# Kernel optimization log

Hardware: AMD Instinct MI355X
Metric: run time of the kernel (lower is better)

Reference implementation:

```python
import jax, jax.numpy as jnp
import numpy as np

B, T, C = 2, 4096, 768
N_HEAD = 12
HEAD_DIM = C // N_HEAD


def setup_inputs() -> dict:
    key = jax.random.key(0)
    k1, k2, k3, k4, k5 = jax.random.split(key, 5)
    scale = 1.0 / np.sqrt(C)
    x = jax.random.normal(k1, (B, T, C), dtype=jnp.float32)
    # weights stored as [in, out] (transpose of torch Linear weight)
    W_attn = jax.random.normal(k2, (C, 3 * C), dtype=jnp.float32) * scale
    b_attn = jax.random.normal(k3, (3 * C,), dtype=jnp.float32) * 0.01
    W_proj = jax.random.normal(k4, (C, C), dtype=jnp.float32) * scale
    b_proj = jax.random.normal(k5, (C,), dtype=jnp.float32) * 0.01
    return {"x": x, "W_attn": W_attn, "b_attn": b_attn, "W_proj": W_proj, "b_proj": b_proj}


def reference(x, W_attn, b_attn, W_proj, b_proj):
    Bq, Tq, Cq = x.shape
    qkv = x @ W_attn + b_attn                      # [B, T, 3C]
    q, k, v = jnp.split(qkv, 3, axis=-1)           # each [B, T, C]

    def heads(t):
        return t.reshape(Bq, Tq, N_HEAD, HEAD_DIM).transpose(0, 2, 1, 3)  # [B, H, T, D]

    q, k, v = heads(q), heads(k), heads(v)
    att = jnp.einsum('bhqd,bhkd->bhqk', q, k) * (1.0 / np.sqrt(HEAD_DIM))  # [B, H, T, T]
    causal = jnp.tril(jnp.ones((Tq, Tq), dtype=bool))                      # [T, T]
    att = jnp.where(causal[None, None], att, jnp.finfo(att.dtype).min)
    att = jax.nn.softmax(att, axis=-1)
    y = jnp.einsum('bhqk,bhkd->bhqd', att, v)      # [B, H, T, D]
    y = y.transpose(0, 2, 1, 3).reshape(Bq, Tq, Cq)
    return y @ W_proj + b_proj
```

## Files before the change

kernel.cpp:

```cpp
#include <hip/hip_runtime.h>


#define TSEQ   4096
#define NHEAD  12
#define CDIM   768
#define C3     2304
#define BT_TOT 8192

#define PSTR   72

typedef __bf16 bf16x8 __attribute__((ext_vector_type(8)));
typedef __bf16 bf16x2 __attribute__((ext_vector_type(2)));
typedef float  f32x4  __attribute__((ext_vector_type(4)));

__device__ __forceinline__ unsigned short f2bf(float f) {
  unsigned int u = __builtin_bit_cast(unsigned int, f);
  u += 0x7FFFu + ((u >> 16) & 1u);
  return (unsigned short)(u >> 16);
}

__device__ __forceinline__ unsigned int pack2bf(float a, float b) {
  bf16x2 v = {(__bf16)a, (__bf16)b};
  return __builtin_bit_cast(unsigned int, v);
}

__device__ __forceinline__ f32x4 mfma16(bf16x8 a, bf16x8 b, f32x4 c) {
  return __builtin_amdgcn_mfma_f32_16x16x32_bf16(a, b, c, 0, 0, 0);
}

typedef const __attribute__((address_space(1))) void* gas_ptr;
typedef __attribute__((address_space(3))) void* las_ptr;

#define LGKM_WAIT() __builtin_amdgcn_s_waitcnt(0xC07F)


__global__ __launch_bounds__(256) void cast_f32_bf16(const float* __restrict__ x,
                                                     unsigned short* __restrict__ o, int n) {
  int i = (blockIdx.x * 256 + threadIdx.x) * 4;
  if (i < n) {
    float4 v = *(const float4*)(x + i);
    ushort4 u;
    u.x = f2bf(v.x); u.y = f2bf(v.y); u.z = f2bf(v.z); u.w = f2bf(v.w);
    *(ushort4*)(o + i) = u;
  }
}

__global__ __launch_bounds__(256) void transpose_cast(const float* __restrict__ src,
                                                      unsigned short* __restrict__ dst,
                                                      int K, int N) {
  __shared__ float tile[32][33];
  int n0 = blockIdx.x * 32, k0 = blockIdx.y * 32;
  int tx = threadIdx.x, ty = threadIdx.y;
#pragma unroll
  for (int i = 0; i < 4; ++i)
    tile[ty + i * 8][tx] = src[(size_t)(k0 + ty + i * 8) * N + n0 + tx];
  __syncthreads();
#pragma unroll
  for (int i = 0; i < 4; ++i)
    dst[(size_t)(n0 + ty + i * 8) * K + k0 + tx] = f2bf(tile[tx][ty + i * 8]);
}


__device__ __forceinline__ void gemm_bt_mainloop(const unsigned short* __restrict__ A,
                                                 const unsigned short* __restrict__ BTm,
                                                 int K, int m0, int n0,
                                                 unsigned short* lds, f32x4 acc[4][4]) {
  const int tid = threadIdx.x;
  const int wave = tid >> 6, lane = tid & 63;
  const int quad = lane >> 4, l16 = lane & 15;
  const int wm = (wave >> 1) * 64, wn = (wave & 1) * 64;
  const int srow = tid >> 2;
  const int scol = (tid & 3) * 8;

  for (int k0 = 0; k0 < K; k0 += 32) {
    __syncthreads();
#pragma unroll
    for (int r = 0; r < 2; ++r) {
      const unsigned short* ga = A + (size_t)(m0 + r * 64 + srow) * K + k0 + scol;
      __builtin_amdgcn_global_load_lds((gas_ptr)ga,
          (las_ptr)(lds + r * 2048 + wave * 512), 16, 0, 0);
      const unsigned short* gb = BTm + (size_t)(n0 + r * 64 + srow) * K + k0 + scol;
      __builtin_amdgcn_global_load_lds((gas_ptr)gb,
          (las_ptr)(lds + 4096 + r * 2048 + wave * 512), 16, 0, 0);
    }
    __syncthreads();

    bf16x8 af[4], bfr[4];
#pragma unroll
    for (int i = 0; i < 4; ++i) {
      af[i]  = *(const bf16x8*)(lds + (wm + i * 16 + l16) * 32 + quad * 8);
      bfr[i] = *(const bf16x8*)(lds + 4096 + (wn + i * 16 + l16) * 32 + quad * 8);
    }
#pragma unroll
    for (int i = 0; i < 4; ++i)
#pragma unroll
      for (int j = 0; j < 4; ++j)
        acc[i][j] = mfma16(af[i], bfr[j], acc[i][j]);
  }
}

__global__ __launch_bounds__(256) void gemm_qkv_kernel(
    const unsigned short* __restrict__ A, const unsigned short* __restrict__ BTm,
    const float* __restrict__ bias,
    unsigned short* __restrict__ qbuf, unsigned short* __restrict__ kbuf,
    unsigned short* __restrict__ vtbuf) {
  __shared__ __align__(16) unsigned short lds[128 * 136];
  f32x4 zero = {0.f, 0.f, 0.f, 0.f};
  f32x4 acc[4][4];
#pragma unroll
  for (int i = 0; i < 4; ++i)
#pragma unroll
    for (int j = 0; j < 4; ++j) acc[i][j] = zero;

  const int m0 = blockIdx.y * 128, n0 = blockIdx.x * 128;
  gemm_bt_mainloop(A, BTm, CDIM, m0, n0, lds, acc);

  const int tid = threadIdx.x;
  const int wave = tid >> 6, lane = tid & 63;
  const int quad = lane >> 4, l16 = lane & 15;
  const int wm = (wave >> 1) * 64, wn = (wave & 1) * 64;
  const float KSCALE = 0.125f * 1.44269504088896340736f;

  const int seg = n0 / CDIM;
  const float mult = (seg == 1) ? KSCALE : 1.0f;

  __syncthreads();
#pragma unroll
  for (int j = 0; j < 4; ++j) {
    const int nl = wn + j * 16 + l16;
    const float bv = bias[n0 + nl];
#pragma unroll
    for (int i = 0; i < 4; ++i) {
#pragma unroll
      for (int r = 0; r < 4; ++r) {
        const int ml = wm + i * 16 + quad * 4 + r;
        unsigned short val = f2bf((acc[i][j][r] + bv) * mult);
        if (seg < 2) lds[ml * 136 + nl] = val;
        else         lds[nl * 136 + ml] = val;
      }
    }
  }
  __syncthreads();

  const int row = tid >> 1, half = tid & 1;
  const unsigned short* src = lds + row * 136 + half * 64;
  unsigned short* dst;
  if (seg < 2) {
    const int m = m0 + row, b = m >> 12, t = m & (TSEQ - 1);
    const int nn = (n0 - seg * CDIM) + half * 64;
    const int h = nn >> 6;
    unsigned short* base = (seg == 0) ? qbuf : kbuf;
    dst = base + ((size_t)(b * NHEAD + h) * TSEQ + t) * 64;
  } else {
    const int nn = (n0 - 2 * CDIM) + row;
    const int h = nn >> 6, d = nn & 63;
    const int b = m0 >> 12, t0 = (m0 & (TSEQ - 1)) + half * 64;
    dst = vtbuf + ((size_t)(b * NHEAD + h) * 64 + d) * TSEQ + t0;
  }
#pragma unroll
  for (int k = 0; k < 8; ++k)
    *(uint4*)(dst + k * 8) = *(const uint4*)(src + k * 8);
}

__global__ __launch_bounds__(256) void gemm_out_kernel(
    const unsigned short* __restrict__ A, const unsigned short* __restrict__ BTm,
    const float* __restrict__ bias, float* __restrict__ out) {
  __shared__ __align__(16) unsigned short lds[8192];
  f32x4 zero = {0.f, 0.f, 0.f, 0.f};
  f32x4 acc[4][4];
#pragma unroll
  for (int i = 0; i < 4; ++i)
#pragma unroll
    for (int j = 0; j < 4; ++j) acc[i][j] = zero;

  const int m0 = blockIdx.y * 128, n0 = blockIdx.x * 128;
  gemm_bt_mainloop(A, BTm, CDIM, m0, n0, lds, acc);

  const int tid = threadIdx.x;
  const int wave = tid >> 6, lane = tid & 63;
  const int quad = lane >> 4, l16 = lane & 15;
  const int wm = (wave >> 1) * 64, wn = (wave & 1) * 64;

#pragma unroll
  for (int j = 0; j < 4; ++j) {
    int n = n0 + wn + j * 16 + l16;
    float bv = bias[n];
#pragma unroll
    for (int i = 0; i < 4; ++i) {
#pragma unroll
      for (int r = 0; r < 4; ++r) {
        int m = m0 + wm + i * 16 + quad * 4 + r;
        out[(size_t)m * CDIM + n] = acc[i][j][r] + bv;
      }
    }
  }
}


__device__ __forceinline__ void stage_kv4(const unsigned short* __restrict__ Kp,
                                          const unsigned short* __restrict__ Vp,
                                          int j0, unsigned short* kb, unsigned short* vb,
                                          int tid, int wave) {
  const int row = tid >> 3;
  const int col = ((tid & 7) ^ (row & 7)) * 8;
  __builtin_amdgcn_global_load_lds((gas_ptr)(Kp + (size_t)(j0 + row) * 64 + col),
                                   (las_ptr)(kb + wave * 512), 16, 0, 0);
  __builtin_amdgcn_global_load_lds((gas_ptr)(Kp + (size_t)(j0 + 32 + row) * 64 + col),
                                   (las_ptr)(kb + 2048 + wave * 512), 16, 0, 0);
  __builtin_amdgcn_global_load_lds((gas_ptr)(Vp + (size_t)row * TSEQ + j0 + col),
                                   (las_ptr)(vb + wave * 512), 16, 0, 0);
  __builtin_amdgcn_global_load_lds((gas_ptr)(Vp + (size_t)(row + 32) * TSEQ + j0 + col),
                                   (las_ptr)(vb + 2048 + wave * 512), 16, 0, 0);
}

__device__ __forceinline__ void qk_score(const bf16x8 kf[8], const bf16x8 qf[2], f32x4 s[4]) {
  f32x4 zero = {0.f, 0.f, 0.f, 0.f};
#pragma unroll
  for (int i = 0; i < 4; ++i)
    s[i] = mfma16(kf[2 * i + 1], qf[1], mfma16(kf[2 * i], qf[0], zero));
}

template <bool MASKED>
__device__ __forceinline__ void exp_write(const f32x4 s[4], unsigned short* __restrict__ prow,
                                          int j0, int q0, int l16, int quad, float& lsum) {
#pragma unroll
  for (int i = 0; i < 4; ++i) {
    float p[4];
#pragma unroll
    for (int r = 0; r < 4; ++r) {
      p[r] = __builtin_amdgcn_exp2f(s[i][r]);
      if (MASKED) {
        if (j0 + i * 16 + quad * 4 + r > q0 + l16) p[r] = 0.f;
      }
      lsum += p[r];
    }
    uint2 w;
    w.x = pack2bf(p[0], p[1]);
    w.y = pack2bf(p[2], p[3]);
    *(uint2*)(prow + l16 * PSTR + i * 16 + quad * 4) = w;
  }
}

__device__ __forceinline__ void pv8(const unsigned short* __restrict__ vb, int kcol0,
                                    const unsigned short* __restrict__ prow,
                                    int l16, int quad, f32x4 o[4]) {
  bf16x8 pf0 = *(const bf16x8*)(prow + l16 * PSTR + quad * 8);
  bf16x8 pf1 = *(const bf16x8*)(prow + l16 * PSTR + 32 + quad * 8);
#pragma unroll
  for (int dt = 0; dt < 4; ++dt) {
    bf16x8 v0 = *(const bf16x8*)(vb + (16 * dt + l16) * 64 + kcol0);
    bf16x8 v1 = *(const bf16x8*)(vb + (16 * dt + l16) * 64 + (kcol0 ^ 32));
    o[dt] = mfma16(pf1, v1, mfma16(pf0, v0, o[dt]));
  }
}

__global__ __launch_bounds__(256, 3) void attn_kernel(const unsigned short* __restrict__ qbuf,
                                                      const unsigned short* __restrict__ kbuf,
                                                      const unsigned short* __restrict__ vtbuf,
                                                      unsigned short* __restrict__ y) {
  __shared__ __align__(16) unsigned short k_lds[2][64 * 64];
  __shared__ __align__(16) unsigned short v_lds[2][64 * 64];
  __shared__ __align__(16) unsigned short p_lds[4][2][16 * PSTR];

  const int tid = threadIdx.x;
  const int wave = tid >> 6, lane = tid & 63;
  const int quad = lane >> 4, l16 = lane & 15;

  const int bh = blockIdx.x % 24;
  const int p = blockIdx.x / 24;
  const int qA0 = p * 64 + wave * 16;
  const int qB0 = (63 - p) * 64 + wave * 16;

  const unsigned short* Qp = qbuf + (size_t)bh * TSEQ * 64;
  const unsigned short* Kp = kbuf + (size_t)bh * TSEQ * 64;
  const unsigned short* Vp = vtbuf + (size_t)bh * 64 * TSEQ;
  unsigned short* prowA = &p_lds[wave][0][0];
  unsigned short* prowB = &p_lds[wave][1][0];

  bf16x8 qfA[2], qfB[2];
  qfA[0] = *(const bf16x8*)(Qp + (size_t)(qA0 + l16) * 64 + quad * 8);
  qfA[1] = *(const bf16x8*)(Qp + (size_t)(qA0 + l16) * 64 + 32 + quad * 8);
  qfB[0] = *(const bf16x8*)(Qp + (size_t)(qB0 + l16) * 64 + quad * 8);
  qfB[1] = *(const bf16x8*)(Qp + (size_t)(qB0 + l16) * 64 + 32 + quad * 8);

  f32x4 zero = {0.f, 0.f, 0.f, 0.f};
  f32x4 oA[4], oB[4];
#pragma unroll
  for (int dt = 0; dt < 4; ++dt) { oA[dt] = zero; oB[dt] = zero; }
  float lsA = 0.f, lsB = 0.f;

  const int kcol0 = (quad ^ (l16 & 7)) * 8;
  const int ntiles = 64 - p;

  stage_kv4(Kp, Vp, 0, k_lds[0], v_lds[0], tid, wave);

  for (int jt = 0; jt < ntiles; ++jt) {
    __syncthreads();
    if (jt + 1 < ntiles)
      stage_kv4(Kp, Vp, (jt + 1) * 64, k_lds[(jt + 1) & 1], v_lds[(jt + 1) & 1], tid, wave);

    const unsigned short* kb = k_lds[jt & 1];
    const unsigned short* vb = v_lds[jt & 1];
    const int j0 = jt * 64;
    const bool actA = jt <= p;

    bf16x8 kf[8];
#pragma unroll
    for (int i = 0; i < 4; ++i) {
      kf[2 * i]     = *(const bf16x8*)(kb + (16 * i + l16) * 64 + kcol0);
      kf[2 * i + 1] = *(const bf16x8*)(kb + (16 * i + l16) * 64 + (kcol0 ^ 32));
    }

    f32x4 sA[4], sB[4];
    if (actA) {
      qk_score(kf, qfA, sA);
      if (jt == p) exp_write<true>(sA, prowA, j0, qA0, l16, quad, lsA);
      else         exp_write<false>(sA, prowA, j0, qA0, l16, quad, lsA);
    }
    qk_score(kf, qfB, sB);
    if (jt == ntiles - 1) exp_write<true>(sB, prowB, j0, qB0, l16, quad, lsB);
    else                  exp_write<false>(sB, prowB, j0, qB0, l16, quad, lsB);

    LGKM_WAIT();

    if (actA) pv8(vb, kcol0, prowA, l16, quad, oA);
    pv8(vb, kcol0, prowB, l16, quad, oB);
  }

  lsA += __shfl_xor(lsA, 16); lsA += __shfl_xor(lsA, 32);
  lsB += __shfl_xor(lsB, 16); lsB += __shfl_xor(lsB, 32);

  const int b = bh / NHEAD, h = bh - b * NHEAD;
#pragma unroll
  for (int r = 0; r < 4; ++r) {
    const int qrow = quad * 4 + r;
    float lqA = __shfl(lsA, (lane & 48) + qrow);
    float lqB = __shfl(lsB, (lane & 48) + qrow);
    float invA = 1.0f / lqA, invB = 1.0f / lqB;
    size_t rowA = (size_t)(b * TSEQ + qA0 + qrow) * CDIM + h * 64;
    size_t rowB = (size_t)(b * TSEQ + qB0 + qrow) * CDIM + h * 64;
#pragma unroll
    for (int dt = 0; dt < 4; ++dt) {
      y[rowA + dt * 16 + l16] = f2bf(oA[dt][r] * invA);
      y[rowB + dt * 16 + l16] = f2bf(oB[dt][r] * invB);
    }
  }
}


extern "C" void kernel_launch(void* const* d_in, const int* in_sizes, int n_in,
                              void* d_out, int out_size, void* d_ws, size_t ws_size,
                              hipStream_t stream) {
  const float* x      = (const float*)d_in[0];
  const float* W_attn = (const float*)d_in[1];
  const float* b_attn = (const float*)d_in[2];
  const float* W_proj = (const float*)d_in[3];
  const float* b_proj = (const float*)d_in[4];
  float* out = (float*)d_out;

  unsigned short* xb    = (unsigned short*)d_ws;
  unsigned short* WaT   = xb + (size_t)BT_TOT * CDIM;
  unsigned short* WpT   = WaT + (size_t)C3 * CDIM;
  unsigned short* qbuf  = WpT + (size_t)CDIM * CDIM;
  unsigned short* kbuf  = qbuf + (size_t)2 * NHEAD * TSEQ * 64;
  unsigned short* vtbuf = kbuf + (size_t)2 * NHEAD * TSEQ * 64;
  unsigned short* ybuf  = xb;

  cast_f32_bf16<<<(BT_TOT * CDIM) / 1024, 256, 0, stream>>>(x, xb, BT_TOT * CDIM);
  transpose_cast<<<dim3(C3 / 32, CDIM / 32), dim3(32, 8), 0, stream>>>(W_attn, WaT, CDIM, C3);
  transpose_cast<<<dim3(CDIM / 32, CDIM / 32), dim3(32, 8), 0, stream>>>(W_proj, WpT, CDIM, CDIM);

  gemm_qkv_kernel<<<dim3(C3 / 128, BT_TOT / 128), 256, 0, stream>>>(xb, WaT, b_attn,
                                                                    qbuf, kbuf, vtbuf);
  attn_kernel<<<dim3(24 * 32), 256, 0, stream>>>(qbuf, kbuf, vtbuf, ybuf);
  gemm_out_kernel<<<dim3(CDIM / 128, BT_TOT / 128), 256, 0, stream>>>(ybuf, WpT, b_proj, out);
}
```

Measured before the change: 241.4 us.

## Use 64-wide K tiles with XOR swizzle in GEMMs; compute softmax row sums via MFMA

The shared GEMM mainloop now stages 64-element K slices with an XOR-swizzled LDS layout and runs two MFMA sub-steps per barrier pair. This halves the number of synchronizations per tile and avoids LDS bank conflicts, at the cost of doubling LDS use in the output GEMM. In attention, the per-lane scalar accumulation of softmax row sums and the shuffle reduction are replaced by an MFMA against a ones vector on the bf16 P tile. V fragments are also loaded once per tile and shared by both query halves. The row sums are now taken from bf16-rounded probabilities, which slightly changes the normalization.

```diff
diff --git a/kernel.cpp b/kernel.cpp
--- a/kernel.cpp
+++ b/kernel.cpp
@@ -61,41 +61,44 @@
 }
 
 
-__device__ __forceinline__ void gemm_bt_mainloop(const unsigned short* __restrict__ A,
-                                                 const unsigned short* __restrict__ BTm,
-                                                 int K, int m0, int n0,
-                                                 unsigned short* lds, f32x4 acc[4][4]) {
+__device__ __forceinline__ void gemm_bt_mainloop64(const unsigned short* __restrict__ A,
+                                                   const unsigned short* __restrict__ BTm,
+                                                   int K, int m0, int n0,
+                                                   unsigned short* lds, f32x4 acc[4][4]) {
   const int tid = threadIdx.x;
   const int wave = tid >> 6, lane = tid & 63;
   const int quad = lane >> 4, l16 = lane & 15;
   const int wm = (wave >> 1) * 64, wn = (wave & 1) * 64;
-  const int srow = tid >> 2;
-  const int scol = (tid & 3) * 8;
-
-  for (int k0 = 0; k0 < K; k0 += 32) {
+  const int srow = lane >> 3;
+  const int scol = ((lane & 7) ^ srow) * 8;
+
+  for (int k0 = 0; k0 < K; k0 += 64) {
     __syncthreads();
 #pragma unroll
-    for (int r = 0; r < 2; ++r) {
-      const unsigned short* ga = A + (size_t)(m0 + r * 64 + srow) * K + k0 + scol;
-      __builtin_amdgcn_global_load_lds((gas_ptr)ga,
-          (las_ptr)(lds + r * 2048 + wave * 512), 16, 0, 0);
-      const unsigned short* gb = BTm + (size_t)(n0 + r * 64 + srow) * K + k0 + scol;
-      __builtin_amdgcn_global_load_lds((gas_ptr)gb,
-          (las_ptr)(lds + 4096 + r * 2048 + wave * 512), 16, 0, 0);
+    for (int c = 0; c < 4; ++c) {
+      const int grow = c * 32 + wave * 8 + srow;
+      __builtin_amdgcn_global_load_lds((gas_ptr)(A + (size_t)(m0 + grow) * K + k0 + scol),
+                                       (las_ptr)(lds + c * 2048 + wave * 512), 16, 0, 0);
+      __builtin_amdgcn_global_load_lds((gas_ptr)(BTm + (size_t)(n0 + grow) * K + k0 + scol),
+                                       (las_ptr)(lds + 8192 + c * 2048 + wave * 512), 16, 0, 0);
     }
     __syncthreads();
 
-    bf16x8 af[4], bfr[4];
-#pragma unroll
-    for (int i = 0; i < 4; ++i) {
-      af[i]  = *(const bf16x8*)(lds + (wm + i * 16 + l16) * 32 + quad * 8);
-      bfr[i] = *(const bf16x8*)(lds + 4096 + (wn + i * 16 + l16) * 32 + quad * 8);
-    }
-#pragma unroll
-    for (int i = 0; i < 4; ++i)
-#pragma unroll
-      for (int j = 0; j < 4; ++j)
-        acc[i][j] = mfma16(af[i], bfr[j], acc[i][j]);
+#pragma unroll
+    for (int kk = 0; kk < 2; ++kk) {
+      const int chunk = ((kk * 4 + quad) ^ (l16 & 7)) * 8;
+      bf16x8 af[4], bfr[4];
+#pragma unroll
+      for (int i = 0; i < 4; ++i) {
+        af[i]  = *(const bf16x8*)(lds + (wm + i * 16 + l16) * 64 + chunk);
+        bfr[i] = *(const bf16x8*)(lds + 8192 + (wn + i * 16 + l16) * 64 + chunk);
+      }
+#pragma unroll
+      for (int i = 0; i < 4; ++i)
+#pragma unroll
+        for (int j = 0; j < 4; ++j)
+          acc[i][j] = mfma16(af[i], bfr[j], acc[i][j]);
+    }
   }
 }
 
@@ -113,7 +116,7 @@
     for (int j = 0; j < 4; ++j) acc[i][j] = zero;
 
   const int m0 = blockIdx.y * 128, n0 = blockIdx.x * 128;
-  gemm_bt_mainloop(A, BTm, CDIM, m0, n0, lds, acc);
+  gemm_bt_mainloop64(A, BTm, CDIM, m0, n0, lds, acc);
 
   const int tid = threadIdx.x;
   const int wave = tid >> 6, lane = tid & 63;
@@ -165,7 +168,7 @@
 __global__ __launch_bounds__(256) void gemm_out_kernel(
     const unsigned short* __restrict__ A, const unsigned short* __restrict__ BTm,
     const float* __restrict__ bias, float* __restrict__ out) {
-  __shared__ __align__(16) unsigned short lds[8192];
+  __shared__ __align__(16) unsigned short lds[16384];
   f32x4 zero = {0.f, 0.f, 0.f, 0.f};
   f32x4 acc[4][4];
 #pragma unroll
@@ -174,7 +177,7 @@
     for (int j = 0; j < 4; ++j) acc[i][j] = zero;
 
   const int m0 = blockIdx.y * 128, n0 = blockIdx.x * 128;
-  gemm_bt_mainloop(A, BTm, CDIM, m0, n0, lds, acc);
+  gemm_bt_mainloop64(A, BTm, CDIM, m0, n0, lds, acc);
 
   const int tid = threadIdx.x;
   const int wave = tid >> 6, lane = tid & 63;
@@ -222,7 +225,7 @@
 
 template <bool MASKED>
 __device__ __forceinline__ void exp_write(const f32x4 s[4], unsigned short* __restrict__ prow,
-                                          int j0, int q0, int l16, int quad, float& lsum) {
+                                          int j0, int q0, int l16, int quad) {
 #pragma unroll
   for (int i = 0; i < 4; ++i) {
     float p[4];
@@ -232,25 +235,11 @@
       if (MASKED) {
         if (j0 + i * 16 + quad * 4 + r > q0 + l16) p[r] = 0.f;
       }
-      lsum += p[r];
     }
     uint2 w;
     w.x = pack2bf(p[0], p[1]);
     w.y = pack2bf(p[2], p[3]);
     *(uint2*)(prow + l16 * PSTR + i * 16 + quad * 4) = w;
-  }
-}
-
-__device__ __forceinline__ void pv8(const unsigned short* __restrict__ vb, int kcol0,
-                                    const unsigned short* __restrict__ prow,
-                                    int l16, int quad, f32x4 o[4]) {
-  bf16x8 pf0 = *(const bf16x8*)(prow + l16 * PSTR + quad * 8);
-  bf16x8 pf1 = *(const bf16x8*)(prow + l16 * PSTR + 32 + quad * 8);
-#pragma unroll
-  for (int dt = 0; dt < 4; ++dt) {
-    bf16x8 v0 = *(const bf16x8*)(vb + (16 * dt + l16) * 64 + kcol0);
-    bf16x8 v1 = *(const bf16x8*)(vb + (16 * dt + l16) * 64 + (kcol0 ^ 32));
-    o[dt] = mfma16(pf1, v1, mfma16(pf0, v0, o[dt]));
   }
 }
 
@@ -283,11 +272,13 @@
   qfB[0] = *(const bf16x8*)(Qp + (size_t)(qB0 + l16) * 64 + quad * 8);
   qfB[1] = *(const bf16x8*)(Qp + (size_t)(qB0 + l16) * 64 + 32 + quad * 8);
 
+  const bf16x8 ones = {(__bf16)1.f, (__bf16)1.f, (__bf16)1.f, (__bf16)1.f,
+                       (__bf16)1.f, (__bf16)1.f, (__bf16)1.f, (__bf16)1.f};
+
   f32x4 zero = {0.f, 0.f, 0.f, 0.f};
-  f32x4 oA[4], oB[4];
+  f32x4 oA[4], oB[4], lA = zero, lB = zero;
 #pragma unroll
   for (int dt = 0; dt < 4; ++dt) { oA[dt] = zero; oB[dt] = zero; }
-  float lsA = 0.f, lsB = 0.f;
 
   const int kcol0 = (quad ^ (l16 & 7)) * 8;
   const int ntiles = 64 - p;
@@ -314,29 +305,45 @@
     f32x4 sA[4], sB[4];
     if (actA) {
       qk_score(kf, qfA, sA);
-      if (jt == p) exp_write<true>(sA, prowA, j0, qA0, l16, quad, lsA);
-      else         exp_write<false>(sA, prowA, j0, qA0, l16, quad, lsA);
+      if (jt == p) exp_write<true>(sA, prowA, j0, qA0, l16, quad);
+      else         exp_write<false>(sA, prowA, j0, qA0, l16, quad);
     }
     qk_score(kf, qfB, sB);
-    if (jt == ntiles - 1) exp_write<true>(sB, prowB, j0, qB0, l16, quad, lsB);
-    else                  exp_write<false>(sB, prowB, j0, qB0, l16, quad, lsB);
+    if (jt == ntiles - 1) exp_write<true>(sB, prowB, j0, qB0, l16, quad);
+    else                  exp_write<false>(sB, prowB, j0, qB0, l16, quad);
 
     LGKM_WAIT();
 
-    if (actA) pv8(vb, kcol0, prowA, l16, quad, oA);
-    pv8(vb, kcol0, prowB, l16, quad, oB);
-  }
-
-  lsA += __shfl_xor(lsA, 16); lsA += __shfl_xor(lsA, 32);
-  lsB += __shfl_xor(lsB, 16); lsB += __shfl_xor(lsB, 32);
+    bf16x8 vf[8];
+#pragma unroll
+    for (int dt = 0; dt < 4; ++dt) {
+      vf[2 * dt]     = *(const bf16x8*)(vb + (16 * dt + l16) * 64 + kcol0);
+      vf[2 * dt + 1] = *(const bf16x8*)(vb + (16 * dt + l16) * 64 + (kcol0 ^ 32));
+    }
+
+    if (actA) {
+      bf16x8 pf0 = *(const bf16x8*)(prowA + l16 * PSTR + quad * 8);
+      bf16x8 pf1 = *(const bf16x8*)(prowA + l16 * PSTR + 32 + quad * 8);
+      lA = mfma16(pf1, ones, mfma16(pf0, ones, lA));
+#pragma unroll
+      for (int dt = 0; dt < 4; ++dt)
+        oA[dt] = mfma16(pf1, vf[2 * dt + 1], mfma16(pf0, vf[2 * dt], oA[dt]));
+    }
+    {
+      bf16x8 pf0 = *(const bf16x8*)(prowB + l16 * PSTR + quad * 8);
+      bf16x8 pf1 = *(const bf16x8*)(prowB + l16 * PSTR + 32 + quad * 8);
+      lB = mfma16(pf1, ones, mfma16(pf0, ones, lB));
+#pragma unroll
+      for (int dt = 0; dt < 4; ++dt)
+        oB[dt] = mfma16(pf1, vf[2 * dt + 1], mfma16(pf0, vf[2 * dt], oB[dt]));
+    }
+  }
 
   const int b = bh / NHEAD, h = bh - b * NHEAD;
 #pragma unroll
   for (int r = 0; r < 4; ++r) {
     const int qrow = quad * 4 + r;
-    float lqA = __shfl(lsA, (lane & 48) + qrow);
-    float lqB = __shfl(lsB, (lane & 48) + qrow);
-    float invA = 1.0f / lqA, invB = 1.0f / lqB;
+    float invA = 1.0f / lA[r], invB = 1.0f / lB[r];
     size_t rowA = (size_t)(b * TSEQ + qA0 + qrow) * CDIM + h * 64;
     size_t rowB = (size_t)(b * TSEQ + qB0 + qrow) * CDIM + h * 64;
 #pragma unroll
```

Result: no change. 243.5 us (+0.9%).
